# Kernel optimization log

Hardware: AMD Instinct MI355X
Metric: run time of the kernel (lower is better)

## Reference

```python
import jax, jax.numpy as jnp
import numpy as np

N_NODES = 100000
N_EDGES = 1600000
IN_DIM = 128
OUT_DIM = 128
N_HEADS = 4


def setup_inputs() -> dict:
    key = jax.random.key(0)
    k1, k2, k3, k4, k5 = jax.random.split(key, 5)
    h = jax.random.normal(k1, (N_NODES, IN_DIM), dtype=jnp.float32)
    src = jax.random.randint(k2, (N_EDGES,), 0, N_NODES, dtype=jnp.int32)
    dst = jax.random.randint(k3, (N_EDGES,), 0, N_NODES, dtype=jnp.int32)
    s = 1.0 / np.sqrt(IN_DIM)
    W_self = jax.random.normal(k4, (N_HEADS, IN_DIM, OUT_DIM), dtype=jnp.float32) * s
    W_neigh = jax.random.normal(k5, (N_HEADS, IN_DIM, OUT_DIM), dtype=jnp.float32) * s
    b = jnp.zeros((N_HEADS, OUT_DIM), dtype=jnp.float32)
    return {"h": h, "src": src, "dst": dst, "W_self": W_self, "W_neigh": W_neigh, "b": b}


def reference(h, src, dst, W_self, W_neigh, b):
    # Mean neighbor aggregation (shared across heads: SAGEConv 'mean' aggregates
    # raw features, then applies per-head linear layers).
    neigh_sum = jax.ops.segment_sum(h[src], dst, num_segments=N_NODES)   # [N, d_in]
    deg = jax.ops.segment_sum(jnp.ones_like(src, dtype=h.dtype), dst,
                              num_segments=N_NODES)                      # [N]
    h_neigh = neigh_sum / jnp.maximum(deg, 1.0)[:, None]                  # [N, d_in]

    # Per-head: fc_self(h_dst) + fc_neigh(h_neigh) + bias -> [H, N, d_out]
    out = (jnp.einsum('nd,hdo->hno', h, W_self)
           + jnp.einsum('nd,hdo->hno', h_neigh, W_neigh)
           + b[:, None, :])
    # merge='mean': average heads
    return jnp.mean(out, axis=0)  # [N, d_out]
```

## Files before the change

kernel.cpp:

```cpp
#include <hip/hip_runtime.h>

#define N_NODES 100000
#define N_EDGES 1600000
#define DIM 128
#define NH 4

#define NPB 512
#define NB 196
#define CAP 12288
#define BCHUNK 8192
#define BEPT 32
#define NBLK ((N_EDGES + BCHUNK - 1) / BCHUNK)

typedef __attribute__((ext_vector_type(8))) short bf16x8;
typedef __attribute__((ext_vector_type(4))) float f32x4;
typedef __attribute__((ext_vector_type(2))) float f32x2;
typedef __attribute__((ext_vector_type(8))) unsigned short u16x8;

#define B_BCUR   0u
#define B_ROWOFF 4096u
#define B_CSR    405504u
#define B_WPACK  6805504u
#define B_BAVG   6871040u
#define B_H8     6871552u
#define NEED_BF16 32869376ull

__device__ inline unsigned short f2bf(float x) {
    union { float f; unsigned u; } v; v.f = x;
    unsigned r = v.u + 0x7fffu + ((v.u >> 16) & 1u);
    return (unsigned short)(r >> 16);
}

__device__ inline void acc_fp8(float (&a)[16], uint4 v) {
    f32x2 r;
    r = __builtin_amdgcn_cvt_pk_f32_fp8((int)v.x, false); a[0] += r[0]; a[1] += r[1];
    r = __builtin_amdgcn_cvt_pk_f32_fp8((int)v.x, true);  a[2] += r[0]; a[3] += r[1];
    r = __builtin_amdgcn_cvt_pk_f32_fp8((int)v.y, false); a[4] += r[0]; a[5] += r[1];
    r = __builtin_amdgcn_cvt_pk_f32_fp8((int)v.y, true);  a[6] += r[0]; a[7] += r[1];
    r = __builtin_amdgcn_cvt_pk_f32_fp8((int)v.z, false); a[8] += r[0]; a[9] += r[1];
    r = __builtin_amdgcn_cvt_pk_f32_fp8((int)v.z, true);  a[10] += r[0]; a[11] += r[1];
    r = __builtin_amdgcn_cvt_pk_f32_fp8((int)v.w, false); a[12] += r[0]; a[13] += r[1];
    r = __builtin_amdgcn_cvt_pk_f32_fp8((int)v.w, true);  a[14] += r[0]; a[15] += r[1];
}

__device__ inline void acc_f32(float (&a)[16], const float4* p) {
    float4 x0 = p[0], x1 = p[1], x2 = p[2], x3 = p[3];
    a[0] += x0.x; a[1] += x0.y; a[2] += x0.z; a[3] += x0.w;
    a[4] += x1.x; a[5] += x1.y; a[6] += x1.z; a[7] += x1.w;
    a[8] += x2.x; a[9] += x2.y; a[10] += x2.z; a[11] += x2.w;
    a[12] += x3.x; a[13] += x3.y; a[14] += x3.z; a[15] += x3.w;
}

template <bool F8>
__global__ __launch_bounds__(256) void prep_kernel(
    const float* __restrict__ h, unsigned char* __restrict__ h8,
    const float* __restrict__ Ws, const float* __restrict__ Wn,
    const float* __restrict__ b, unsigned short* __restrict__ wpack,
    float* __restrict__ bavg, int* __restrict__ bcur) {
    const int t = threadIdx.x;
    if (blockIdx.x == 0) bcur[t] = t * CAP;
    int i = blockIdx.x * 256 + t;
    if (i < DIM * DIM) {
        float s = 0.f, n = 0.f;
#pragma unroll
        for (int hh = 0; hh < NH; ++hh) {
            s += Ws[hh * DIM * DIM + i];
            n += Wn[hh * DIM * DIM + i];
        }
        s *= 0.25f; n *= 0.25f;
        int k = i >> 7, o = i & 127;
        int nt = o >> 4, lanelo = o & 15;
        int ks = k >> 5, lanehi = (k & 31) >> 3, e = k & 7;
        int pos = (((nt * 4 + ks) * 64) + lanehi * 16 + lanelo) * 8 + e;
        wpack[pos] = f2bf(s);
        wpack[16384 + pos] = f2bf(n);
    }
    if (i < DIM) {
        float bb = 0.f;
#pragma unroll
        for (int hh = 0; hh < NH; ++hh) bb += b[hh * DIM + i];
        bavg[i] = 0.25f * bb;
    }
    if (F8) {
        const float4* p = reinterpret_cast<const float4*>(h) + (size_t)i * 2;
        float4 a = p[0], c = p[1];
        int d0 = 0, d1 = 0;
        d0 = __builtin_amdgcn_cvt_pk_fp8_f32(a.x, a.y, d0, false);
        d0 = __builtin_amdgcn_cvt_pk_fp8_f32(a.z, a.w, d0, true);
        d1 = __builtin_amdgcn_cvt_pk_fp8_f32(c.x, c.y, d1, false);
        d1 = __builtin_amdgcn_cvt_pk_fp8_f32(c.z, c.w, d1, true);
        reinterpret_cast<uint2*>(h8)[i] = make_uint2((unsigned)d0, (unsigned)d1);
    }
}

__global__ __launch_bounds__(256) void bucket_scatter_kernel(const int* __restrict__ src,
                                                             const int* __restrict__ dst,
                                                             int* __restrict__ bcur,
                                                             int* __restrict__ ebuf) {
    __shared__ int stage[BCHUNK];
    __shared__ unsigned char bkt[BCHUNK];
    __shared__ int lc[256], lbase[256], lpos[256];
    int t = threadIdx.x;
    lc[t] = 0;
    lpos[t] = 0;
    __syncthreads();
    int e0 = blockIdx.x * BCHUNK;
#pragma unroll 4
    for (int j = 0; j < BEPT; ++j) {
        int e = e0 + j * 256 + t;
        if (e < N_EDGES) {
            int d = dst[e];
            stage[j * 256 + t] = (src[e] << 9) | (d & (NPB - 1));
            bkt[j * 256 + t] = (unsigned char)(d >> 9);
            atomicAdd(&lc[d >> 9], 1);
        }
    }
    __syncthreads();
    if (lc[t]) lbase[t] = atomicAdd(&bcur[t], lc[t]);
    __syncthreads();
#pragma unroll 4
    for (int j = 0; j < BEPT; ++j) {
        int e = e0 + j * 256 + t;
        if (e < N_EDGES) {
            int bb = bkt[j * 256 + t];
            int o = atomicAdd(&lpos[bb], 1);
            ebuf[lbase[bb] + o] = stage[j * 256 + t];
        }
    }
}

__global__ __launch_bounds__(256) void csr_build_kernel(const int* __restrict__ bcur,
                                                        const int* __restrict__ ebuf,
                                                        int* __restrict__ rowoff,
                                                        int* __restrict__ csr) {
    __shared__ int hh[NPB], off[NPB], cur[NPB], ss[256];
    int b = blockIdx.x, t = threadIdx.x;
    int cnt = bcur[b] - b * CAP;
    int ibase = b * CAP;
    ss[t] = bcur[t] - t * CAP;
    __syncthreads();
    for (int o = 1; o < 256; o <<= 1) {
        int add = (t >= o) ? ss[t - o] : 0;
        __syncthreads();
        ss[t] += add;
        __syncthreads();
    }
    int obase = ss[b] - cnt;
    hh[t] = 0; hh[t + 256] = 0;
    cur[t] = 0; cur[t + 256] = 0;
    __syncthreads();
    for (int i = t; i < cnt; i += 256) atomicAdd(&hh[ebuf[ibase + i] & (NPB - 1)], 1);
    __syncthreads();
    int e0 = hh[2 * t], e1 = hh[2 * t + 1];
    ss[t] = e0 + e1;
    __syncthreads();
    for (int o = 1; o < 256; o <<= 1) {
        int add = (t >= o) ? ss[t - o] : 0;
        __syncthreads();
        ss[t] += add;
        __syncthreads();
    }
    int ex = ss[t] - (e0 + e1);
    off[2 * t] = ex;
    off[2 * t + 1] = ex + e0;
    __syncthreads();
    int n0 = b * NPB;
#pragma unroll
    for (int k = 0; k < 2; ++k) {
        int s2 = 2 * t + k;
        int n = n0 + s2;
        int dgv = (k == 0) ? e0 : e1;
        if (n < N_NODES) rowoff[n] = ((obase + off[s2]) << 9) | min(dgv, 511);
    }
    for (int i = t; i < cnt; i += 256) {
        int p = ebuf[ibase + i];
        int nl = p & (NPB - 1);
        int o = atomicAdd(&cur[nl], 1);
        csr[obase + off[nl] + o] = p >> 9;
    }
}

template <bool F8>
__global__ __launch_bounds__(256) void gather_mean_kernel(
    const float* __restrict__ h, const unsigned char* __restrict__ h8,
    const int* __restrict__ rowoff, const int* __restrict__ csr,
    float* __restrict__ out) {
    const int node = blockIdx.x * 4 + (threadIdx.x >> 6);
    const int lane = threadIdx.x & 63;
    const int s = lane >> 3;
    const int c = lane & 7;
    const int w = rowoff[node];
    const int lo = w >> 9, dg = w & 511, hi = lo + dg;
    float a[16];
#pragma unroll
    for (int i = 0; i < 16; ++i) a[i] = 0.f;
    if (F8 && dg >= 8) {
        int k = lo + s;
        for (; k + 8 < hi; k += 16) {
            int s0 = csr[k], s1 = csr[k + 8];
            uint4 v = *reinterpret_cast<const uint4*>(h8 + (size_t)s0 * DIM + c * 16);
            uint4 u = *reinterpret_cast<const uint4*>(h8 + (size_t)s1 * DIM + c * 16);
            acc_fp8(a, v);
            acc_fp8(a, u);
        }
        for (; k < hi; k += 8) {
            uint4 v = *reinterpret_cast<const uint4*>(h8 + (size_t)csr[k] * DIM + c * 16);
            acc_fp8(a, v);
        }
    } else {
        for (int k = lo + s; k < hi; k += 8)
            acc_f32(a, reinterpret_cast<const float4*>(h + (size_t)csr[k] * DIM + c * 16));
    }
#pragma unroll
    for (int i = 0; i < 16; ++i) {
        a[i] += __shfl_xor(a[i], 8, 64);
        a[i] += __shfl_xor(a[i], 16, 64);
        a[i] += __shfl_xor(a[i], 32, 64);
    }
    float inv = 1.0f / (float)max(dg, 1);
    if (s == 0) {
        if (F8) {
            u16x8 r0, r1;
#pragma unroll
            for (int j = 0; j < 8; ++j) {
                r0[j] = f2bf(a[j] * inv);
                r1[j] = f2bf(a[8 + j] * inv);
            }
            unsigned short* base = reinterpret_cast<unsigned short*>(out) + (size_t)node * 256 + c * 16;
            *reinterpret_cast<u16x8*>(base) = r0;
            *reinterpret_cast<u16x8*>(base + 8) = r1;
        } else {
            float4* q = reinterpret_cast<float4*>(out + (size_t)node * DIM + c * 16);
            q[0] = make_float4(a[0] * inv, a[1] * inv, a[2] * inv, a[3] * inv);
            q[1] = make_float4(a[4] * inv, a[5] * inv, a[6] * inv, a[7] * inv);
            q[2] = make_float4(a[8] * inv, a[9] * inv, a[10] * inv, a[11] * inv);
            q[3] = make_float4(a[12] * inv, a[13] * inv, a[14] * inv, a[15] * inv);
        }
    }
}

template <bool F8>
__global__ __launch_bounds__(256) void mfma_gemm_kernel(
    const float* __restrict__ h, float* __restrict__ out,
    const unsigned short* __restrict__ wpack, const float* __restrict__ bavg) {
    const int lane = threadIdx.x & 63;
    const int wid = threadIdx.x >> 6;
    const int node_base = blockIdx.x * 64 + wid * 16;
    const int row = node_base + (lane & 15);
    const int rowc = min(row, N_NODES - 1);
    const int khi = lane >> 4;

    f32x4 acc[8] = {};
    const unsigned short* wn_p = wpack + 16384;

#pragma unroll
    for (int ks = 0; ks < 4; ++ks) {
        const int k0 = ks * 32 + khi * 8;
        bf16x8 ha, na;
        const float4* hp = reinterpret_cast<const float4*>(h + (size_t)rowc * DIM + k0);
        float4 x = hp[0], y = hp[1];
        ha[0] = (short)f2bf(x.x); ha[1] = (short)f2bf(x.y);
        ha[2] = (short)f2bf(x.z); ha[3] = (short)f2bf(x.w);
        ha[4] = (short)f2bf(y.x); ha[5] = (short)f2bf(y.y);
        ha[6] = (short)f2bf(y.z); ha[7] = (short)f2bf(y.w);
        if (F8) {
            na = *reinterpret_cast<const bf16x8*>(
                reinterpret_cast<const unsigned short*>(out) + (size_t)rowc * 256 + k0);
        } else {
            const float4* np0 = reinterpret_cast<const float4*>(out + (size_t)rowc * DIM + k0);
            float4 u = np0[0], v = np0[1];
            na[0] = (short)f2bf(u.x); na[1] = (short)f2bf(u.y);
            na[2] = (short)f2bf(u.z); na[3] = (short)f2bf(u.w);
            na[4] = (short)f2bf(v.x); na[5] = (short)f2bf(v.y);
            na[6] = (short)f2bf(v.z); na[7] = (short)f2bf(v.w);
        }

#pragma unroll
        for (int nt = 0; nt < 8; ++nt) {
            bf16x8 bs = *reinterpret_cast<const bf16x8*>(wpack + (size_t)(((nt * 4 + ks) * 64 + lane) * 8));
            acc[nt] = __builtin_amdgcn_mfma_f32_16x16x32_bf16(ha, bs, acc[nt], 0, 0, 0);
            bf16x8 bn = *reinterpret_cast<const bf16x8*>(wn_p + (size_t)(((nt * 4 + ks) * 64 + lane) * 8));
            acc[nt] = __builtin_amdgcn_mfma_f32_16x16x32_bf16(na, bn, acc[nt], 0, 0, 0);
        }
    }

    const int r0 = node_base + khi * 4;
#pragma unroll
    for (int nt = 0; nt < 8; ++nt) {
        int o = nt * 16 + (lane & 15);
        float bb = bavg[o];
#pragma unroll
        for (int r = 0; r < 4; ++r) {
            int nr = r0 + r;
            if (nr < N_NODES) out[(size_t)nr * DIM + o] = acc[nt][r] + bb;
        }
    }
}

extern "C" void kernel_launch(void* const* d_in, const int* in_sizes, int n_in,
                              void* d_out, int out_size, void* d_ws, size_t ws_size,
                              hipStream_t stream) {
    const float* h  = (const float*)d_in[0];
    const int* src  = (const int*)d_in[1];
    const int* dst  = (const int*)d_in[2];
    const float* Ws = (const float*)d_in[3];
    const float* Wn = (const float*)d_in[4];
    const float* b  = (const float*)d_in[5];
    float* out = (float*)d_out;

    char* ws = (char*)d_ws;
    int* bcur   = (int*)(ws + B_BCUR);
    int* rowoff = (int*)(ws + B_ROWOFF);
    int* csr    = (int*)(ws + B_CSR);
    unsigned short* wpack = (unsigned short*)(ws + B_WPACK);
    float* bavg = (float*)(ws + B_BAVG);
    unsigned char* h8 = (unsigned char*)(ws + B_H8);
    int* ebuf   = (int*)d_out;

    const bool f8 = (ws_size >= NEED_BF16);

    if (f8)
        prep_kernel<true><<<(N_NODES * DIM / 8) / 256, 256, 0, stream>>>(h, h8, Ws, Wn, b, wpack, bavg, bcur);
    else
        prep_kernel<false><<<64, 256, 0, stream>>>(h, h8, Ws, Wn, b, wpack, bavg, bcur);
    bucket_scatter_kernel<<<NBLK, 256, 0, stream>>>(src, dst, bcur, ebuf);
    csr_build_kernel<<<NB, 256, 0, stream>>>(bcur, ebuf, rowoff, csr);
    if (f8)
        gather_mean_kernel<true><<<N_NODES / 4, 256, 0, stream>>>(h, h8, rowoff, csr, out);
    else
        gather_mean_kernel<false><<<N_NODES / 4, 256, 0, stream>>>(h, h8, rowoff, csr, out);
    const int gemm_blocks = (N_NODES + 63) / 64;
    if (f8)
        mfma_gemm_kernel<true><<<gemm_blocks, 256, 0, stream>>>(h, out, wpack, bavg);
    else
        mfma_gemm_kernel<false><<<gemm_blocks, 256, 0, stream>>>(h, out, wpack, bavg);
}
```

Before: 146.8 us.

## Merge prep into bucket scatter kernel and make gather grid-stride

Folds the weight-averaging, bias averaging and fp8 conversion of h into extra blocks of the bucket scatter kernel, so the two independent phases run concurrently in one launch. The bucket counters are zeroed by a memset and hold relative counts, with the per-bucket base added at use. The gather kernel becomes a persistent grid-stride loop over a fixed number of blocks instead of one block per four nodes. This saves one kernel launch and lets the scatter overlap the conversion, at the cost of an added memset launch and possible load imbalance in the fixed-size gather grid.

```diff
diff --git a/kernel.cpp b/kernel.cpp
--- a/kernel.cpp
+++ b/kernel.cpp
@@ -11,6 +11,8 @@
 #define BCHUNK 8192
 #define BEPT 32
 #define NBLK ((N_EDGES + BCHUNK - 1) / BCHUNK)
+#define PREP_BLKS 64
+#define GATHER_BLKS 2048
 
 typedef __attribute__((ext_vector_type(8))) short bf16x8;
 typedef __attribute__((ext_vector_type(4))) float f32x4;
@@ -52,55 +54,55 @@
 }
 
 template <bool F8>
-__global__ __launch_bounds__(256) void prep_kernel(
+__global__ __launch_bounds__(256) void prep_scatter_kernel(
+    const int* __restrict__ src, const int* __restrict__ dst,
+    int* __restrict__ bcur, int* __restrict__ ebuf,
     const float* __restrict__ h, unsigned char* __restrict__ h8,
     const float* __restrict__ Ws, const float* __restrict__ Wn,
     const float* __restrict__ b, unsigned short* __restrict__ wpack,
-    float* __restrict__ bavg, int* __restrict__ bcur) {
+    float* __restrict__ bavg) {
     const int t = threadIdx.x;
-    if (blockIdx.x == 0) bcur[t] = t * CAP;
-    int i = blockIdx.x * 256 + t;
-    if (i < DIM * DIM) {
-        float s = 0.f, n = 0.f;
-#pragma unroll
-        for (int hh = 0; hh < NH; ++hh) {
-            s += Ws[hh * DIM * DIM + i];
-            n += Wn[hh * DIM * DIM + i];
-        }
-        s *= 0.25f; n *= 0.25f;
-        int k = i >> 7, o = i & 127;
-        int nt = o >> 4, lanelo = o & 15;
-        int ks = k >> 5, lanehi = (k & 31) >> 3, e = k & 7;
-        int pos = (((nt * 4 + ks) * 64) + lanehi * 16 + lanelo) * 8 + e;
-        wpack[pos] = f2bf(s);
-        wpack[16384 + pos] = f2bf(n);
-    }
-    if (i < DIM) {
-        float bb = 0.f;
-#pragma unroll
-        for (int hh = 0; hh < NH; ++hh) bb += b[hh * DIM + i];
-        bavg[i] = 0.25f * bb;
-    }
-    if (F8) {
-        const float4* p = reinterpret_cast<const float4*>(h) + (size_t)i * 2;
-        float4 a = p[0], c = p[1];
-        int d0 = 0, d1 = 0;
-        d0 = __builtin_amdgcn_cvt_pk_fp8_f32(a.x, a.y, d0, false);
-        d0 = __builtin_amdgcn_cvt_pk_fp8_f32(a.z, a.w, d0, true);
-        d1 = __builtin_amdgcn_cvt_pk_fp8_f32(c.x, c.y, d1, false);
-        d1 = __builtin_amdgcn_cvt_pk_fp8_f32(c.z, c.w, d1, true);
-        reinterpret_cast<uint2*>(h8)[i] = make_uint2((unsigned)d0, (unsigned)d1);
-    }
-}
-
-__global__ __launch_bounds__(256) void bucket_scatter_kernel(const int* __restrict__ src,
-                                                             const int* __restrict__ dst,
-                                                             int* __restrict__ bcur,
-                                                             int* __restrict__ ebuf) {
+    if (blockIdx.x >= NBLK) {
+        const int wid = blockIdx.x - NBLK;
+        int i = wid * 256 + t;
+        if (i < DIM * DIM) {
+            float s = 0.f, n = 0.f;
+#pragma unroll
+            for (int hh = 0; hh < NH; ++hh) {
+                s += Ws[hh * DIM * DIM + i];
+                n += Wn[hh * DIM * DIM + i];
+            }
+            s *= 0.25f; n *= 0.25f;
+            int k = i >> 7, o = i & 127;
+            int nt = o >> 4, lanelo = o & 15;
+            int ks = k >> 5, lanehi = (k & 31) >> 3, e = k & 7;
+            int pos = (((nt * 4 + ks) * 64) + lanehi * 16 + lanelo) * 8 + e;
+            wpack[pos] = f2bf(s);
+            wpack[16384 + pos] = f2bf(n);
+        }
+        if (i < DIM) {
+            float bb = 0.f;
+#pragma unroll
+            for (int hh = 0; hh < NH; ++hh) bb += b[hh * DIM + i];
+            bavg[i] = 0.25f * bb;
+        }
+        if (F8) {
+            for (int c8 = i; c8 < N_NODES * DIM / 8; c8 += PREP_BLKS * 256) {
+                const float4* p = reinterpret_cast<const float4*>(h) + (size_t)c8 * 2;
+                float4 a = p[0], c = p[1];
+                int d0 = 0, d1 = 0;
+                d0 = __builtin_amdgcn_cvt_pk_fp8_f32(a.x, a.y, d0, false);
+                d0 = __builtin_amdgcn_cvt_pk_fp8_f32(a.z, a.w, d0, true);
+                d1 = __builtin_amdgcn_cvt_pk_fp8_f32(c.x, c.y, d1, false);
+                d1 = __builtin_amdgcn_cvt_pk_fp8_f32(c.z, c.w, d1, true);
+                reinterpret_cast<uint2*>(h8)[c8] = make_uint2((unsigned)d0, (unsigned)d1);
+            }
+        }
+        return;
+    }
     __shared__ int stage[BCHUNK];
     __shared__ unsigned char bkt[BCHUNK];
     __shared__ int lc[256], lbase[256], lpos[256];
-    int t = threadIdx.x;
     lc[t] = 0;
     lpos[t] = 0;
     __syncthreads();
@@ -116,7 +118,7 @@
         }
     }
     __syncthreads();
-    if (lc[t]) lbase[t] = atomicAdd(&bcur[t], lc[t]);
+    if (lc[t]) lbase[t] = t * CAP + atomicAdd(&bcur[t], lc[t]);
     __syncthreads();
 #pragma unroll 4
     for (int j = 0; j < BEPT; ++j) {
@@ -135,9 +137,9 @@
                                                         int* __restrict__ csr) {
     __shared__ int hh[NPB], off[NPB], cur[NPB], ss[256];
     int b = blockIdx.x, t = threadIdx.x;
-    int cnt = bcur[b] - b * CAP;
+    int cnt = bcur[b];
     int ibase = b * CAP;
-    ss[t] = bcur[t] - t * CAP;
+    ss[t] = bcur[t];
     __syncthreads();
     for (int o = 1; o < 256; o <<= 1) {
         int add = (t >= o) ? ss[t - o] : 0;
@@ -185,56 +187,58 @@
     const float* __restrict__ h, const unsigned char* __restrict__ h8,
     const int* __restrict__ rowoff, const int* __restrict__ csr,
     float* __restrict__ out) {
-    const int node = blockIdx.x * 4 + (threadIdx.x >> 6);
     const int lane = threadIdx.x & 63;
     const int s = lane >> 3;
     const int c = lane & 7;
-    const int w = rowoff[node];
-    const int lo = w >> 9, dg = w & 511, hi = lo + dg;
-    float a[16];
-#pragma unroll
-    for (int i = 0; i < 16; ++i) a[i] = 0.f;
-    if (F8 && dg >= 8) {
-        int k = lo + s;
-        for (; k + 8 < hi; k += 16) {
-            int s0 = csr[k], s1 = csr[k + 8];
-            uint4 v = *reinterpret_cast<const uint4*>(h8 + (size_t)s0 * DIM + c * 16);
-            uint4 u = *reinterpret_cast<const uint4*>(h8 + (size_t)s1 * DIM + c * 16);
-            acc_fp8(a, v);
-            acc_fp8(a, u);
-        }
-        for (; k < hi; k += 8) {
-            uint4 v = *reinterpret_cast<const uint4*>(h8 + (size_t)csr[k] * DIM + c * 16);
-            acc_fp8(a, v);
-        }
-    } else {
-        for (int k = lo + s; k < hi; k += 8)
-            acc_f32(a, reinterpret_cast<const float4*>(h + (size_t)csr[k] * DIM + c * 16));
-    }
-#pragma unroll
-    for (int i = 0; i < 16; ++i) {
-        a[i] += __shfl_xor(a[i], 8, 64);
-        a[i] += __shfl_xor(a[i], 16, 64);
-        a[i] += __shfl_xor(a[i], 32, 64);
-    }
-    float inv = 1.0f / (float)max(dg, 1);
-    if (s == 0) {
-        if (F8) {
-            u16x8 r0, r1;
-#pragma unroll
-            for (int j = 0; j < 8; ++j) {
-                r0[j] = f2bf(a[j] * inv);
-                r1[j] = f2bf(a[8 + j] * inv);
-            }
-            unsigned short* base = reinterpret_cast<unsigned short*>(out) + (size_t)node * 256 + c * 16;
-            *reinterpret_cast<u16x8*>(base) = r0;
-            *reinterpret_cast<u16x8*>(base + 8) = r1;
+    for (int node = blockIdx.x * 4 + (threadIdx.x >> 6); node < N_NODES;
+         node += GATHER_BLKS * 4) {
+        const int w = rowoff[node];
+        const int lo = w >> 9, dg = w & 511, hi = lo + dg;
+        float a[16];
+#pragma unroll
+        for (int i = 0; i < 16; ++i) a[i] = 0.f;
+        if (F8 && dg >= 8) {
+            int k = lo + s;
+            for (; k + 8 < hi; k += 16) {
+                int s0 = csr[k], s1 = csr[k + 8];
+                uint4 v = *reinterpret_cast<const uint4*>(h8 + (size_t)s0 * DIM + c * 16);
+                uint4 u = *reinterpret_cast<const uint4*>(h8 + (size_t)s1 * DIM + c * 16);
+                acc_fp8(a, v);
+                acc_fp8(a, u);
+            }
+            for (; k < hi; k += 8) {
+                uint4 v = *reinterpret_cast<const uint4*>(h8 + (size_t)csr[k] * DIM + c * 16);
+                acc_fp8(a, v);
+            }
         } else {
-            float4* q = reinterpret_cast<float4*>(out + (size_t)node * DIM + c * 16);
-            q[0] = make_float4(a[0] * inv, a[1] * inv, a[2] * inv, a[3] * inv);
-            q[1] = make_float4(a[4] * inv, a[5] * inv, a[6] * inv, a[7] * inv);
-            q[2] = make_float4(a[8] * inv, a[9] * inv, a[10] * inv, a[11] * inv);
-            q[3] = make_float4(a[12] * inv, a[13] * inv, a[14] * inv, a[15] * inv);
+            for (int k = lo + s; k < hi; k += 8)
+                acc_f32(a, reinterpret_cast<const float4*>(h + (size_t)csr[k] * DIM + c * 16));
+        }
+#pragma unroll
+        for (int i = 0; i < 16; ++i) {
+            a[i] += __shfl_xor(a[i], 8, 64);
+            a[i] += __shfl_xor(a[i], 16, 64);
+            a[i] += __shfl_xor(a[i], 32, 64);
+        }
+        float inv = 1.0f / (float)max(dg, 1);
+        if (s == 0) {
+            if (F8) {
+                u16x8 r0, r1;
+#pragma unroll
+                for (int j = 0; j < 8; ++j) {
+                    r0[j] = f2bf(a[j] * inv);
+                    r1[j] = f2bf(a[8 + j] * inv);
+                }
+                unsigned short* base = reinterpret_cast<unsigned short*>(out) + (size_t)node * 256 + c * 16;
+                *reinterpret_cast<u16x8*>(base) = r0;
+                *reinterpret_cast<u16x8*>(base + 8) = r1;
+            } else {
+                float4* q = reinterpret_cast<float4*>(out + (size_t)node * DIM + c * 16);
+                q[0] = make_float4(a[0] * inv, a[1] * inv, a[2] * inv, a[3] * inv);
+                q[1] = make_float4(a[4] * inv, a[5] * inv, a[6] * inv, a[7] * inv);
+                q[2] = make_float4(a[8] * inv, a[9] * inv, a[10] * inv, a[11] * inv);
+                q[3] = make_float4(a[12] * inv, a[13] * inv, a[14] * inv, a[15] * inv);
+            }
         }
     }
 }
@@ -319,16 +323,19 @@
 
     const bool f8 = (ws_size >= NEED_BF16);
 
+    hipMemsetAsync(bcur, 0, 256 * sizeof(int), stream);
+
     if (f8)
-        prep_kernel<true><<<(N_NODES * DIM / 8) / 256, 256, 0, stream>>>(h, h8, Ws, Wn, b, wpack, bavg, bcur);
+        prep_scatter_kernel<true><<<NBLK + PREP_BLKS, 256, 0, stream>>>(
+            src, dst, bcur, ebuf, h, h8, Ws, Wn, b, wpack, bavg);
     else
-        prep_kernel<false><<<64, 256, 0, stream>>>(h, h8, Ws, Wn, b, wpack, bavg, bcur);
-    bucket_scatter_kernel<<<NBLK, 256, 0, stream>>>(src, dst, bcur, ebuf);
+        prep_scatter_kernel<false><<<NBLK + PREP_BLKS, 256, 0, stream>>>(
+            src, dst, bcur, ebuf, h, h8, Ws, Wn, b, wpack, bavg);
     csr_build_kernel<<<NB, 256, 0, stream>>>(bcur, ebuf, rowoff, csr);
     if (f8)
-        gather_mean_kernel<true><<<N_NODES / 4, 256, 0, stream>>>(h, h8, rowoff, csr, out);
+        gather_mean_kernel<true><<<GATHER_BLKS, 256, 0, stream>>>(h, h8, rowoff, csr, out);
     else
-        gather_mean_kernel<false><<<N_NODES / 4, 256, 0, stream>>>(h, h8, rowoff, csr, out);
+        gather_mean_kernel<false><<<GATHER_BLKS, 256, 0, stream>>>(h, h8, rowoff, csr, out);
     const int gemm_blocks = (N_NODES + 63) / 64;
     if (f8)
         mfma_gemm_kernel<true><<<gemm_blocks, 256, 0, stream>>>(h, out, wpack, bavg);
```

New measurement: 175.5 us. 1.2x slower.
